# Kernel tuning notes

Hardware: AMD Instinct MI355X
Metric: run time of the kernel (lower is better)

## Reference

```python
import jax, jax.numpy as jnp
import numpy as np

B, N, DEG = 32, 1024, 8
E = B * N * DEG
NT = B * N
F_IN, HID, EDIM, NR, HD = 64, 128, 16, 16, 4
NEG = 0.2  # leaky_relu negative slope (alpha)
K1 = int(np.ceil(0.8 * N))    # 820 kept nodes per graph after pool1
K2 = int(np.ceil(0.8 * K1))   # 656 kept nodes per graph after pool2


def setup_inputs() -> dict:
    key = jax.random.key(0)
    ks = jax.random.split(key, 20)
    nrm = lambda i, shp, s=0.05: jax.random.normal(ks[i], shp, jnp.float32) * s
    x = jax.random.normal(ks[0], (NT, F_IN), jnp.float32)
    off = (jnp.arange(B) * N)[:, None]
    src = (jax.random.randint(ks[1], (B, N * DEG), 0, N) + off).reshape(-1)
    dst = (jax.random.randint(ks[2], (B, N * DEG), 0, N) + off).reshape(-1)
    edge_index = jnp.stack([src, dst]).astype(jnp.int32)
    edge_attr = jax.random.normal(ks[3], (E, EDIM), jnp.float32)
    action = jax.random.normal(ks[4], (B, NR), jnp.float32)
    return dict(
        x=x, edge_attr=edge_attr, action=action,
        W1l=nrm(5, (F_IN, HD * HID)), b1l=jnp.zeros(HD * HID),
        W1r=nrm(6, (F_IN, HD * HID)), b1r=jnp.zeros(HD * HID),
        W1e=nrm(7, (EDIM, HD * HID)), att1=nrm(8, (HD, HID)), bias1=jnp.zeros(HID),
        W2l=nrm(9, (HID, HD * HID)), b2l=jnp.zeros(HD * HID),
        W2r=nrm(10, (HID, HD * HID)), b2r=jnp.zeros(HD * HID),
        W2e=nrm(11, (EDIM, HD * HID)), att2=nrm(12, (HD, HID)), bias2=jnp.zeros(HID),
        p1=nrm(13, (HID,), 0.1), p2=nrm(14, (HID,), 0.1),
        Wf1=nrm(15, (2 * HID + NR, HID)), bf1=jnp.zeros(HID),
        Wf2=nrm(16, (HID, HID)), bf2=jnp.zeros(HID),
        Wf3=nrm(17, (HID, 1), 0.003), bf3=jnp.zeros(1),
        edge_index=edge_index,
    )


def _gatv2(x, edge_index, edge_attr, edge_mask, Wl, bl, Wr, br, We, att, bias):
    # PyG GATv2Conv, concat=False (mean over heads), eval mode (no dropout).
    src, dst = edge_index[0], edge_index[1]
    n = x.shape[0]
    xl = (x @ Wl + bl).reshape(n, HD, HID)   # source transform (x_j)
    xr = (x @ Wr + br).reshape(n, HD, HID)   # target transform (x_i)
    ef = (edge_attr @ We).reshape(-1, HD, HID)
    m = jax.nn.leaky_relu(xl[src] + xr[dst] + ef, NEG)          # [E,H,C]
    logits = jnp.where(edge_mask[:, None], (m * att).sum(-1), -1e9)  # [E,H]
    mx = jax.ops.segment_max(logits, dst, num_segments=n)
    a = jnp.exp(logits - mx[dst])
    den = jax.ops.segment_sum(a, dst, num_segments=n)
    alpha = (a / (den[dst] + 1e-16)) * edge_mask[:, None]       # softmax per dst, masked edges zeroed
    out = jax.ops.segment_sum(xl[src] * alpha[..., None], dst, num_segments=n)
    return out.mean(axis=1) + bias


def _topk(x, node_mask, p, k):
    # PyG TopKPooling: score = x@p/||p||, gate = tanh(score), keep top-k per graph.
    score = (x @ p) / (jnp.linalg.norm(p) + 1e-16)
    gate = jnp.tanh(score)
    s = jnp.where(node_mask, score, -jnp.inf).reshape(B, N)
    idx = jax.lax.top_k(s, k)[1]                                # [B,k]
    keep = jnp.zeros((B, N), bool).at[jnp.arange(B)[:, None], idx].set(True).reshape(-1)
    return x * gate[:, None], keep


def reference(x, edge_attr, action, W1l, b1l, W1r, b1r, W1e, att1, bias1,
              W2l, b2l, W2r, b2r, W2e, att2, bias2, p1, p2,
              Wf1, bf1, Wf2, bf2, Wf3, bf3, edge_index):
    src, dst = edge_index[0], edge_index[1]
    em0 = jnp.ones((E,), bool)
    h = jax.nn.relu(_gatv2(x, edge_index, edge_attr, em0,
                           W1l, b1l, W1r, b1r, W1e, att1, bias1))
    h, keep1 = _topk(h, jnp.ones((NT,), bool), p1, K1)
    em1 = keep1[src] & keep1[dst]
    h = jax.nn.relu(_gatv2(h, edge_index, edge_attr, em1,
                           W2l, b2l, W2r, b2r, W2e, att2, bias2))
    h, keep2 = _topk(h, keep1, p2, K2)
    hb = h.reshape(B, N, HID)
    mb = keep2.reshape(B, N)[..., None]
    gmx = jnp.where(mb, hb, -jnp.inf).max(axis=1)               # global max pool over kept nodes
    gav = (hb * mb).sum(axis=1) / K2                            # global mean pool (K2 kept per graph)
    z = jnp.concatenate([gmx, gav, action], axis=1)             # [B, 2*HID+NR]
    z = jax.nn.relu(z @ Wf1 + bf1)
    z = jax.nn.relu(z @ Wf2 + bf2)
    return z @ Wf3 + bf3
```

## Files before the change

kernel.cpp:

```cpp
#include <hip/hip_runtime.h>
#include <math.h>

#define NTN 32768
#define NBG 32
#define NN  1024
#define EE  262144
#define FIN 64
#define HIDC 128
#define HD  4
#define HC  512
#define EDIM 16
#define NR  16
#define KP1 820
#define KP2 656
#define NKEPT (KP1 * NBG)
#define NEGS 0.2f
#define NPB 2
#define SHIFT 10.0f
#define EPAD (EE + 3 * NTN + 64)

template<int K>
__global__ __launch_bounds__(256) void gemm_node3(const float* __restrict__ A,
                                                  const float* __restrict__ Wl,
                                                  const float* __restrict__ bl,
                                                  const float* __restrict__ Wr,
                                                  const float* __restrict__ br,
                                                  const float* __restrict__ gs,
                                                  const int* __restrict__ ids,
                                                  float* __restrict__ Cl,
                                                  float* __restrict__ Cr) {
    __shared__ float a_s[64][K];
    __shared__ int rid_s[64];
    __shared__ float g_s[64];
    int t = threadIdx.x;
    int rb = blockIdx.x >> 2, cg = blockIdx.x & 3;
    int row0 = rb * 64;
    if (t < 64) {
        int rid = ids ? ids[row0 + t] : (row0 + t);
        rid_s[t] = rid;
        g_s[t] = gs ? tanhf(gs[rid]) : 1.0f;
    }
    __syncthreads();
    for (int i = t; i < 64 * K; i += 256) {
        int r = i / K, k = i % K;
        a_s[r][k] = A[(size_t)rid_s[r] * K + k] * g_s[r];
    }
    __syncthreads();
    int tc = cg * 128 + (t & 63) * 2;
    int rg = (t >> 6) * 16;
    float accl0[16], accl1[16], accr0[16], accr1[16];
    float2 blv = *(const float2*)&bl[tc];
    float2 brv = *(const float2*)&br[tc];
    #pragma unroll
    for (int r = 0; r < 16; r++) { accl0[r] = blv.x; accl1[r] = blv.y; accr0[r] = brv.x; accr1[r] = brv.y; }
    for (int k = 0; k < K; k++) {
        float2 wl = *(const float2*)&Wl[(size_t)k * HC + tc];
        float2 wr = *(const float2*)&Wr[(size_t)k * HC + tc];
        #pragma unroll
        for (int r = 0; r < 16; r++) {
            float a = a_s[rg + r][k];
            accl0[r] += a * wl.x; accl1[r] += a * wl.y;
            accr0[r] += a * wr.x; accr1[r] += a * wr.y;
        }
    }
    for (int r = 0; r < 16; r++) {
        size_t base = (size_t)rid_s[rg + r] * HC + tc;
        *(float2*)&Cl[base] = make_float2(accl0[r], accl1[r]);
        *(float2*)&Cr[base] = make_float2(accr0[r], accr1[r]);
    }
}

__global__ void edge_hist(const int* __restrict__ dst, int* __restrict__ deg) {
    int e = blockIdx.x * 256 + threadIdx.x;
    if (e < EE) atomicAdd(&deg[dst[e]], 1);
}

__global__ __launch_bounds__(1024) void scan_deg(const int* __restrict__ deg,
                                                 int* __restrict__ off, int* __restrict__ cur,
                                                 const float* __restrict__ p1,
                                                 const float* __restrict__ p2,
                                                 float* __restrict__ pn) {
    __shared__ int s[1024];
    int t = threadIdx.x;
    int base = t * 32;
    int local[32];
    int sum = 0;
    #pragma unroll
    for (int i = 0; i < 32; i++) { local[i] = (deg[base + i] + 3) & ~3; sum += local[i]; }
    s[t] = sum;
    for (int o = 1; o < 1024; o <<= 1) {
        __syncthreads();
        int v = (t >= o) ? s[t - o] : 0;
        __syncthreads();
        s[t] += v;
    }
    __syncthreads();
    int run = s[t] - sum;
    #pragma unroll
    for (int i = 0; i < 32; i++) { off[base + i] = run; cur[base + i] = run; run += local[i]; }
    if (t == 1023) off[NTN] = s[1023];
    if (t < 64) {
        float a = p1[t] * p1[t] + p1[t + 64] * p1[t + 64];
        float b = p2[t] * p2[t] + p2[t + 64] * p2[t + 64];
        #pragma unroll
        for (int sft = 32; sft; sft >>= 1) { a += __shfl_xor(a, sft, 64); b += __shfl_xor(b, sft, 64); }
        if (t == 0) { pn[0] = 1.f / (sqrtf(a) + 1e-16f); pn[1] = 1.f / (sqrtf(b) + 1e-16f); }
    }
}

__global__ void edge_scatter(const int* __restrict__ dst, const int* __restrict__ src,
                             const float* __restrict__ ea, int* __restrict__ cur,
                             int* __restrict__ esrc, float* __restrict__ eaP) {
    int e = blockIdx.x * 256 + threadIdx.x;
    if (e < EE) {
        int p = atomicAdd(&cur[dst[e]], 1);
        esrc[p] = src[e];
        const float4* s4 = (const float4*)(ea + (size_t)e * EDIM);
        float4* d4 = (float4*)(eaP + (size_t)p * EDIM);
        d4[0] = s4[0]; d4[1] = s4[1]; d4[2] = s4[2]; d4[3] = s4[3];
    }
}

__global__ void pad_fill(const int* __restrict__ cur, const int* __restrict__ off,
                         int* __restrict__ esrc, float* __restrict__ eaP) {
    int d = blockIdx.x * 256 + threadIdx.x;
    if (d < NTN) {
        int p0 = cur[d], p1 = off[d + 1];
        float4 z = make_float4(0.f, 0.f, 0.f, 0.f);
        for (int p = p0; p < p1; p++) {
            esrc[p] = -1;
            float4* d4 = (float4*)(eaP + (size_t)p * EDIM);
            d4[0] = z; d4[1] = z; d4[2] = z; d4[3] = z;
        }
    }
}

__global__ __launch_bounds__(256) void gat_dst(
        const float* __restrict__ xl, const float* __restrict__ xr,
        const float* __restrict__ eaP, const float* __restrict__ We,
        const float* __restrict__ att, const float* __restrict__ bias,
        const float* __restrict__ pvec, const float* __restrict__ pnInv,
        const int* __restrict__ esrc, const int* __restrict__ off,
        const int* __restrict__ keep,
        float* __restrict__ out, float* __restrict__ score, int nblk) {
    int bid = blockIdx.x;
    int swz = (bid & 7) * (nblk >> 3) + (bid >> 3);
    int d0 = swz * NPB;
    int t = threadIdx.x;
    int w = t >> 6, lane = t & 63;
    int c = w * HIDC + lane * 2;
    __shared__ float red[NPB][HC];
    __shared__ float red2[NPB][HIDC];
    float we0[EDIM], we1[EDIM];
    #pragma unroll
    for (int k = 0; k < EDIM; k++) {
        we0[k] = We[k * HC + c];
        we1[k] = We[k * HC + c + 1];
    }
    float at0 = att[c], at1 = att[c + 1];
    const float* xlc = xl + c;

    for (int n = 0; n < NPB; n++) {
        int d = d0 + n;
        float denA = 0.f, aA0 = 0.f, aA1 = 0.f;
        float denB = 0.f, aB0 = 0.f, aB1 = 0.f;
        bool live = (keep == nullptr) || (keep[d] != 0);
        if (live) {
            float2 xrv = *(const float2*)&xr[((size_t)d << 9) + c];
            int e0 = __builtin_amdgcn_readfirstlane(off[d]);
            int e1 = __builtin_amdgcn_readfirstlane(off[d + 1]);
            for (int ei = e0; ei < e1; ei += 4) {
                int s[4]; float msk[4]; float2 xv[4]; float p[4];
                #pragma unroll
                for (int j = 0; j < 4; j++) {
                    int sv = esrc[ei + j];
                    int sc = sv < 0 ? 0 : sv;
                    float mk = (sv >= 0) ? 1.f : 0.f;
                    if (keep && sv >= 0 && !keep[sc]) mk = 0.f;
                    s[j] = sc; msk[j] = mk;
                }
                #pragma unroll
                for (int j = 0; j < 4; j++) xv[j] = *(const float2*)&xlc[(size_t)s[j] << 9];
                #pragma unroll
                for (int j = 0; j < 4; j++) {
                    const float* eap = eaP + (size_t)(ei + j) * EDIM;
                    float ef0 = 0.f, ef1 = 0.f;
                    #pragma unroll
                    for (int k = 0; k < EDIM; k++) {
                        float e = eap[k];
                        ef0 += e * we0[k]; ef1 += e * we1[k];
                    }
                    float v0 = xv[j].x + xrv.x + ef0; v0 = v0 > 0.f ? v0 : NEGS * v0;
                    float v1 = xv[j].y + xrv.y + ef1; v1 = v1 > 0.f ? v1 : NEGS * v1;
                    p[j] = v0 * at0 + v1 * at1;
                }
                #pragma unroll
                for (int sft = 32; sft; sft >>= 1) {
                    #pragma unroll
                    for (int j = 0; j < 4; j++) p[j] += __shfl_xor(p[j], sft, 64);
                }
                float w0 = msk[0] * __expf(p[0] - SHIFT);
                float w1 = msk[1] * __expf(p[1] - SHIFT);
                float w2 = msk[2] * __expf(p[2] - SHIFT);
                float w3 = msk[3] * __expf(p[3] - SHIFT);
                denA += w0; aA0 += w0 * xv[0].x; aA1 += w0 * xv[0].y;
                denB += w1; aB0 += w1 * xv[1].x; aB1 += w1 * xv[1].y;
                denA += w2; aA0 += w2 * xv[2].x; aA1 += w2 * xv[2].y;
                denB += w3; aB0 += w3 * xv[3].x; aB1 += w3 * xv[3].y;
            }
        }
        float inv = 1.f / (denA + denB + 1e-16f);
        red[n][c] = (aA0 + aB0) * inv;
        red[n][c + 1] = (aA1 + aB1) * inv;
    }
    __syncthreads();
    {
        int n2 = t >> 7, tc = t & 127;
        float v = (red[n2][tc] + red[n2][tc + 128] + red[n2][tc + 256] + red[n2][tc + 384]) * 0.25f
                  + bias[tc];
        v = fmaxf(v, 0.f);
        out[((size_t)(d0 + n2) << 7) + tc] = v;
        red2[n2][tc] = v * pvec[tc];
    }
    __syncthreads();
    if (t < 128) {
        int n3 = t >> 6, l2 = t & 63;
        float sv = red2[n3][l2] + red2[n3][l2 + 64];
        #pragma unroll
        for (int sft = 32; sft; sft >>= 1) sv += __shfl_xor(sv, sft, 64);
        if (l2 == 0) score[d0 + n3] = sv * pnInv[0];
    }
}

__global__ __launch_bounds__(512) void topk_sel(const float* __restrict__ score,
                                                const int* __restrict__ mask, int k,
                                                int* __restrict__ keep, int* __restrict__ klist) {
    __shared__ float v[NN];
    __shared__ short id[NN];
    int g = blockIdx.x, t = threadIdx.x;
    for (int i = t; i < NN; i += 512) {
        int n = g * NN + i;
        bool mk = mask ? (mask[n] != 0) : true;
        v[i] = mk ? score[n] : -INFINITY;
        id[i] = (short)i;
    }
    __syncthreads();
    for (int kk = 2; kk <= NN; kk <<= 1) {
        for (int j = kk >> 1; j > 0; j >>= 1) {
            #pragma unroll 2
            for (int i = t; i < NN; i += 512) {
                int ixj = i ^ j;
                if (ixj > i) {
                    bool up = ((i & kk) == 0);
                    float a = v[i], b2 = v[ixj];
                    short ia = id[i], ib = id[ixj];
                    bool aFirst = (a > b2) || (a == b2 && ia < ib);
                    if (up ? !aFirst : aFirst) { v[i] = b2; v[ixj] = a; id[i] = ib; id[ixj] = ia; }
                }
            }
            __syncthreads();
        }
    }
    for (int i = t; i < NN; i += 512) {
        int kp = (i < k) ? 1 : 0;
        keep[g * NN + id[i]] = kp;
        if (klist && kp) klist[g * k + i] = g * NN + id[i];
    }
}

__global__ __launch_bounds__(512) void tail(const float* __restrict__ score,
                                            const int* __restrict__ mask,
                                            const float* __restrict__ h,
                                            const float* __restrict__ action,
                                            const float* __restrict__ Wf1, const float* __restrict__ bf1,
                                            const float* __restrict__ Wf2, const float* __restrict__ bf2,
                                            const float* __restrict__ Wf3, const float* __restrict__ bf3,
                                            float* __restrict__ out) {
    int g = blockIdx.x, t = threadIdx.x;
    __shared__ float v[NN];
    __shared__ short id[NN];
    __shared__ float gt_s[NN];
    __shared__ char kp_s[NN];
    __shared__ float smx[4][HIDC], ssm[4][HIDC];
    __shared__ float zs[2 * HIDC + NR], z1[HIDC], z2[HIDC], rr[HIDC];
    for (int i = t; i < NN; i += 512) {
        int n = g * NN + i;
        bool mk = (mask[n] != 0);
        v[i] = mk ? score[n] : -INFINITY;
        id[i] = (short)i;
        kp_s[i] = 0;
        gt_s[i] = 0.f;
    }
    __syncthreads();
    for (int kk = 2; kk <= NN; kk <<= 1) {
        for (int j = kk >> 1; j > 0; j >>= 1) {
            #pragma unroll 2
            for (int i = t; i < NN; i += 512) {
                int ixj = i ^ j;
                if (ixj > i) {
                    bool up = ((i & kk) == 0);
                    float a = v[i], b2 = v[ixj];
                    short ia = id[i], ib = id[ixj];
                    bool aFirst = (a > b2) || (a == b2 && ia < ib);
                    if (up ? !aFirst : aFirst) { v[i] = b2; v[ixj] = a; id[i] = ib; id[ixj] = ia; }
                }
            }
            __syncthreads();
        }
    }
    for (int i = t; i < NN; i += 512) {
        if (i < KP2) {
            int nid = id[i];
            kp_s[nid] = 1;
            gt_s[nid] = tanhf(score[g * NN + nid]);
        }
    }
    __syncthreads();
    int c = t & 127, ch = t >> 7;
    float mx = -INFINITY, sm = 0.f;
    for (int n = ch * 256; n < ch * 256 + 256; n++) {
        if (kp_s[n]) {
            float hv = h[(size_t)(g * NN + n) * HIDC + c] * gt_s[n];
            mx = fmaxf(mx, hv);
            sm += hv;
        }
    }
    smx[ch][c] = mx; ssm[ch][c] = sm;
    __syncthreads();
    if (t < HIDC) {
        mx = fmaxf(fmaxf(smx[0][t], smx[1][t]), fmaxf(smx[2][t], smx[3][t]));
        sm = ssm[0][t] + ssm[1][t] + ssm[2][t] + ssm[3][t];
        zs[t] = mx;
        zs[HIDC + t] = sm / (float)KP2;
        if (t < NR) zs[2 * HIDC + t] = action[g * NR + t];
    }
    __syncthreads();
    if (t < HIDC) {
        float a = bf1[t];
        for (int k = 0; k < 2 * HIDC + NR; k++) a += zs[k] * Wf1[(size_t)k * HIDC + t];
        z1[t] = fmaxf(a, 0.f);
    }
    __syncthreads();
    if (t < HIDC) {
        float a = bf2[t];
        for (int k = 0; k < HIDC; k++) a += z1[k] * Wf2[(size_t)k * HIDC + t];
        z2[t] = fmaxf(a, 0.f);
        rr[t] = z2[t] * Wf3[t];
    }
    __syncthreads();
    for (int s = 64; s; s >>= 1) {
        if (t < s) rr[t] += rr[t + s];
        __syncthreads();
    }
    if (t == 0) out[g] = rr[0] + bf3[0];
}

extern "C" void kernel_launch(void* const* d_in, const int* in_sizes, int n_in,
                              void* d_out, int out_size, void* d_ws, size_t ws_size,
                              hipStream_t stream) {
    const float* x    = (const float*)d_in[0];
    const float* ea   = (const float*)d_in[1];
    const float* act  = (const float*)d_in[2];
    const float* W1l  = (const float*)d_in[3];
    const float* b1l  = (const float*)d_in[4];
    const float* W1r  = (const float*)d_in[5];
    const float* b1r  = (const float*)d_in[6];
    const float* W1e  = (const float*)d_in[7];
    const float* att1 = (const float*)d_in[8];
    const float* bias1= (const float*)d_in[9];
    const float* W2l  = (const float*)d_in[10];
    const float* b2l  = (const float*)d_in[11];
    const float* W2r  = (const float*)d_in[12];
    const float* b2r  = (const float*)d_in[13];
    const float* W2e  = (const float*)d_in[14];
    const float* att2 = (const float*)d_in[15];
    const float* bias2= (const float*)d_in[16];
    const float* p1   = (const float*)d_in[17];
    const float* p2   = (const float*)d_in[18];
    const float* Wf1  = (const float*)d_in[19];
    const float* bf1  = (const float*)d_in[20];
    const float* Wf2  = (const float*)d_in[21];
    const float* bf2  = (const float*)d_in[22];
    const float* Wf3  = (const float*)d_in[23];
    const float* bf3  = (const float*)d_in[24];
    const int*   eix  = (const int*)d_in[25];
    const int* srcA = eix;
    const int* dstA = eix + EE;

    float* ws    = (float*)d_ws;
    float* xl    = ws;
    float* xr    = xl + (size_t)NTN * HC;
    float* h     = xr + (size_t)NTN * HC;
    float* score1= h + (size_t)NTN * HIDC;
    float* score2= score1 + NTN;
    float* pn    = score2 + NTN;
    int* keep1 = (int*)(pn + 2);
    int* klist = keep1 + NTN;
    int* deg   = klist + NKEPT;
    int* off   = deg + NTN;
    int* cur   = off + NTN + 1;
    int* esrc  = cur + NTN;
    float* eaP  = (float*)(esrc + EPAD);

    hipMemsetAsync(deg, 0, NTN * sizeof(int), stream);
    edge_hist<<<EE / 256, 256, 0, stream>>>(dstA, deg);
    scan_deg<<<1, 1024, 0, stream>>>(deg, off, cur, p1, p2, pn);
    edge_scatter<<<EE / 256, 256, 0, stream>>>(dstA, srcA, ea, cur, esrc, eaP);
    pad_fill<<<NTN / 256, 256, 0, stream>>>(cur, off, esrc, eaP);

    gemm_node3<FIN><<<(NTN / 64) * 4, 256, 0, stream>>>(x, W1l, b1l, W1r, b1r, nullptr, nullptr, xl, xr);
    gat_dst<<<NTN / NPB, 256, 0, stream>>>(xl, xr, eaP, W1e, att1, bias1, p1, pn, esrc, off, nullptr, h, score1, NTN / NPB);

    topk_sel<<<NBG, 512, 0, stream>>>(score1, nullptr, KP1, keep1, klist);

    gemm_node3<HIDC><<<(NKEPT / 64) * 4, 256, 0, stream>>>(h, W2l, b2l, W2r, b2r, score1, klist, xl, xr);
    gat_dst<<<NTN / NPB, 256, 0, stream>>>(xl, xr, eaP, W2e, att2, bias2, p2, pn + 1, esrc, off, keep1, h, score2, NTN / NPB);

    tail<<<NBG, 512, 0, stream>>>(score2, keep1, h, act,
                                  Wf1, bf1, Wf2, bf2, Wf3, bf3, (float*)d_out);
}
```

Baseline: 600.6 us.

## Build per-graph CSR in shared memory, precompute masked sources, use transpose-reduce for logits

Replaces the global histogram, single-block scan, scatter and pad-fill kernels with one per-graph CSR build that uses shared-memory atomics, plus a separate permutation pass for edge attributes. Padding is dropped: tail slots are clamped and masked instead. A precomputed esrc2 array folds the keep1 source mask in before layer 2, so the gather loop no longer reads keep. The four per-edge logit reductions now share one transpose-style shuffle tree instead of four full butterflies, with float4 edge-attribute loads and 32-bit index math. This costs an extra masking kernel and a perm buffer.

```diff
diff --git a/kernel.cpp b/kernel.cpp
--- a/kernel.cpp
+++ b/kernel.cpp
@@ -4,6 +4,7 @@
 #define NTN 32768
 #define NBG 32
 #define NN  1024
+#define EPG 8192
 #define EE  262144
 #define FIN 64
 #define HIDC 128
@@ -17,7 +18,6 @@
 #define NEGS 0.2f
 #define NPB 2
 #define SHIFT 10.0f
-#define EPAD (EE + 3 * NTN + 64)
 
 template<int K>
 __global__ __launch_bounds__(256) void gemm_node3(const float* __restrict__ A,
@@ -70,71 +70,70 @@
     }
 }
 
-__global__ void edge_hist(const int* __restrict__ dst, int* __restrict__ deg) {
-    int e = blockIdx.x * 256 + threadIdx.x;
-    if (e < EE) atomicAdd(&deg[dst[e]], 1);
-}
-
-__global__ __launch_bounds__(1024) void scan_deg(const int* __restrict__ deg,
-                                                 int* __restrict__ off, int* __restrict__ cur,
-                                                 const float* __restrict__ p1,
-                                                 const float* __restrict__ p2,
-                                                 float* __restrict__ pn) {
-    __shared__ int s[1024];
-    int t = threadIdx.x;
-    int base = t * 32;
-    int local[32];
-    int sum = 0;
+__global__ __launch_bounds__(1024) void csr_build(const int* __restrict__ dst,
+                                                  const int* __restrict__ src,
+                                                  int* __restrict__ off,
+                                                  int* __restrict__ esrc,
+                                                  int* __restrict__ perm,
+                                                  const float* __restrict__ p1,
+                                                  const float* __restrict__ p2,
+                                                  float* __restrict__ pn) {
+    int g = blockIdx.x, t = threadIdx.x;
+    __shared__ int degS[NN];
+    __shared__ int scanS[NN];
+    __shared__ int curS[NN];
+    degS[t] = 0;
+    __syncthreads();
+    int eb = g * EPG;
     #pragma unroll
-    for (int i = 0; i < 32; i++) { local[i] = (deg[base + i] + 3) & ~3; sum += local[i]; }
-    s[t] = sum;
-    for (int o = 1; o < 1024; o <<= 1) {
+    for (int i = t; i < EPG; i += 1024) atomicAdd(&degS[dst[eb + i] - g * NN], 1);
+    __syncthreads();
+    int dg = degS[t];
+    scanS[t] = dg;
+    for (int o = 1; o < NN; o <<= 1) {
         __syncthreads();
-        int v = (t >= o) ? s[t - o] : 0;
+        int v = (t >= o) ? scanS[t - o] : 0;
         __syncthreads();
-        s[t] += v;
-    }
-    __syncthreads();
-    int run = s[t] - sum;
-    #pragma unroll
-    for (int i = 0; i < 32; i++) { off[base + i] = run; cur[base + i] = run; run += local[i]; }
-    if (t == 1023) off[NTN] = s[1023];
-    if (t < 64) {
+        scanS[t] += v;
+    }
+    __syncthreads();
+    int excl = scanS[t] - dg;
+    off[g * NN + t] = eb + excl;
+    curS[t] = excl;
+    if (g == NBG - 1 && t == NN - 1) off[NTN] = EE;
+    if (g == 0 && t < 64) {
         float a = p1[t] * p1[t] + p1[t + 64] * p1[t + 64];
         float b = p2[t] * p2[t] + p2[t + 64] * p2[t + 64];
         #pragma unroll
         for (int sft = 32; sft; sft >>= 1) { a += __shfl_xor(a, sft, 64); b += __shfl_xor(b, sft, 64); }
         if (t == 0) { pn[0] = 1.f / (sqrtf(a) + 1e-16f); pn[1] = 1.f / (sqrtf(b) + 1e-16f); }
     }
-}
-
-__global__ void edge_scatter(const int* __restrict__ dst, const int* __restrict__ src,
-                             const float* __restrict__ ea, int* __restrict__ cur,
-                             int* __restrict__ esrc, float* __restrict__ eaP) {
-    int e = blockIdx.x * 256 + threadIdx.x;
-    if (e < EE) {
-        int p = atomicAdd(&cur[dst[e]], 1);
+    __syncthreads();
+    #pragma unroll
+    for (int i = t; i < EPG; i += 1024) {
+        int e = eb + i;
+        int ld = dst[e] - g * NN;
+        int p = eb + atomicAdd(&curS[ld], 1);
         esrc[p] = src[e];
-        const float4* s4 = (const float4*)(ea + (size_t)e * EDIM);
-        float4* d4 = (float4*)(eaP + (size_t)p * EDIM);
-        d4[0] = s4[0]; d4[1] = s4[1]; d4[2] = s4[2]; d4[3] = s4[3];
-    }
-}
-
-__global__ void pad_fill(const int* __restrict__ cur, const int* __restrict__ off,
-                         int* __restrict__ esrc, float* __restrict__ eaP) {
-    int d = blockIdx.x * 256 + threadIdx.x;
-    if (d < NTN) {
-        int p0 = cur[d], p1 = off[d + 1];
-        float4 z = make_float4(0.f, 0.f, 0.f, 0.f);
-        for (int p = p0; p < p1; p++) {
-            esrc[p] = -1;
-            float4* d4 = (float4*)(eaP + (size_t)p * EDIM);
-            d4[0] = z; d4[1] = z; d4[2] = z; d4[3] = z;
-        }
-    }
-}
-
+        perm[p] = e;
+    }
+}
+
+__global__ void ea_permute(const int* __restrict__ perm, const float* __restrict__ ea,
+                           float* __restrict__ eaP) {
+    int id = blockIdx.x * 256 + threadIdx.x;
+    int p = id >> 2, q = id & 3;
+    ((float4*)eaP)[p * 4 + q] = ((const float4*)ea)[perm[p] * 4 + q];
+}
+
+__global__ void esrc_mask(const int* __restrict__ esrc, const int* __restrict__ keep,
+                          int* __restrict__ esrc2) {
+    int i = blockIdx.x * 256 + threadIdx.x;
+    int sv = esrc[i];
+    esrc2[i] = keep[sv] ? sv : -1;
+}
+
+template<bool L2>
 __global__ __launch_bounds__(256) void gat_dst(
         const float* __restrict__ xl, const float* __restrict__ xr,
         const float* __restrict__ eaP, const float* __restrict__ We,
@@ -164,49 +163,61 @@
         int d = d0 + n;
         float denA = 0.f, aA0 = 0.f, aA1 = 0.f;
         float denB = 0.f, aB0 = 0.f, aB1 = 0.f;
-        bool live = (keep == nullptr) || (keep[d] != 0);
+        bool live = !L2 || (keep[d] != 0);
         if (live) {
-            float2 xrv = *(const float2*)&xr[((size_t)d << 9) + c];
+            float2 xrv = *(const float2*)&xr[((unsigned)d << 9) + (unsigned)c];
             int e0 = __builtin_amdgcn_readfirstlane(off[d]);
             int e1 = __builtin_amdgcn_readfirstlane(off[d + 1]);
+            int last = e1 - 1;
             for (int ei = e0; ei < e1; ei += 4) {
-                int s[4]; float msk[4]; float2 xv[4]; float p[4];
+                float mk[4]; float2 xv[4]; float p[4]; int slc[4];
                 #pragma unroll
                 for (int j = 0; j < 4; j++) {
-                    int sv = esrc[ei + j];
-                    int sc = sv < 0 ? 0 : sv;
-                    float mk = (sv >= 0) ? 1.f : 0.f;
-                    if (keep && sv >= 0 && !keep[sc]) mk = 0.f;
-                    s[j] = sc; msk[j] = mk;
+                    int sl = ei + j;
+                    slc[j] = sl <= last ? sl : last;
+                    int sv = esrc[slc[j]];
+                    float m = (sl <= last && sv >= 0) ? 1.f : 0.f;
+                    int sidx = sv >= 0 ? sv : 0;
+                    mk[j] = m;
+                    xv[j] = *(const float2*)(xlc + ((unsigned)sidx << 9));
                 }
                 #pragma unroll
-                for (int j = 0; j < 4; j++) xv[j] = *(const float2*)&xlc[(size_t)s[j] << 9];
-                #pragma unroll
                 for (int j = 0; j < 4; j++) {
-                    const float* eap = eaP + (size_t)(ei + j) * EDIM;
+                    const float4* eap = (const float4*)eaP + ((unsigned)slc[j] << 2);
+                    float4 E0 = eap[0], E1 = eap[1], E2 = eap[2], E3 = eap[3];
+                    float ev[16] = {E0.x, E0.y, E0.z, E0.w, E1.x, E1.y, E1.z, E1.w,
+                                    E2.x, E2.y, E2.z, E2.w, E3.x, E3.y, E3.z, E3.w};
                     float ef0 = 0.f, ef1 = 0.f;
                     #pragma unroll
-                    for (int k = 0; k < EDIM; k++) {
-                        float e = eap[k];
-                        ef0 += e * we0[k]; ef1 += e * we1[k];
-                    }
+                    for (int k = 0; k < EDIM; k++) { ef0 += ev[k] * we0[k]; ef1 += ev[k] * we1[k]; }
                     float v0 = xv[j].x + xrv.x + ef0; v0 = v0 > 0.f ? v0 : NEGS * v0;
                     float v1 = xv[j].y + xrv.y + ef1; v1 = v1 > 0.f ? v1 : NEGS * v1;
                     p[j] = v0 * at0 + v1 * at1;
                 }
-                #pragma unroll
-                for (int sft = 32; sft; sft >>= 1) {
-                    #pragma unroll
-                    for (int j = 0; j < 4; j++) p[j] += __shfl_xor(p[j], sft, 64);
-                }
-                float w0 = msk[0] * __expf(p[0] - SHIFT);
-                float w1 = msk[1] * __expf(p[1] - SHIFT);
-                float w2 = msk[2] * __expf(p[2] - SHIFT);
-                float w3 = msk[3] * __expf(p[3] - SHIFT);
-                denA += w0; aA0 += w0 * xv[0].x; aA1 += w0 * xv[0].y;
-                denB += w1; aB0 += w1 * xv[1].x; aB1 += w1 * xv[1].y;
-                denA += w2; aA0 += w2 * xv[2].x; aA1 += w2 * xv[2].y;
-                denB += w3; aB0 += w3 * xv[3].x; aB1 += w3 * xv[3].y;
+                bool o1 = (lane & 1), o2 = (lane & 2);
+                float a0 = o1 ? p[1] : p[0], b0 = o1 ? p[0] : p[1];
+                float q0 = a0 + __shfl_xor(b0, 1, 64);
+                float a1 = o1 ? p[3] : p[2], b1 = o1 ? p[2] : p[3];
+                float q1 = a1 + __shfl_xor(b1, 1, 64);
+                float a2 = o2 ? q1 : q0, b2 = o2 ? q0 : q1;
+                float r = a2 + __shfl_xor(b2, 2, 64);
+                r += __shfl_xor(r, 4, 64);
+                r += __shfl_xor(r, 8, 64);
+                r += __shfl_xor(r, 16, 64);
+                r += __shfl_xor(r, 32, 64);
+                float s0 = __shfl(r, 0, 64);
+                float s1 = __shfl(r, 1, 64);
+                float s2 = __shfl(r, 2, 64);
+                float s3 = __shfl(r, 3, 64);
+                float w0 = mk[0] * __expf(s0 - SHIFT);
+                float w1 = mk[1] * __expf(s1 - SHIFT);
+                float w2 = mk[2] * __expf(s2 - SHIFT);
+                float w3 = mk[3] * __expf(s3 - SHIFT);
+                denA += w0 + w2; denB += w1 + w3;
+                aA0 += w0 * xv[0].x; aA1 += w0 * xv[0].y;
+                aB0 += w1 * xv[1].x; aB1 += w1 * xv[1].y;
+                aA0 += w2 * xv[2].x; aA1 += w2 * xv[2].y;
+                aB0 += w3 * xv[3].x; aB1 += w3 * xv[3].y;
             }
         }
         float inv = 1.f / (denA + denB + 1e-16f);
@@ -219,7 +230,7 @@
         float v = (red[n2][tc] + red[n2][tc + 128] + red[n2][tc + 256] + red[n2][tc + 384]) * 0.25f
                   + bias[tc];
         v = fmaxf(v, 0.f);
-        out[((size_t)(d0 + n2) << 7) + tc] = v;
+        out[((unsigned)(d0 + n2) << 7) + (unsigned)tc] = v;
         red2[n2][tc] = v * pvec[tc];
     }
     __syncthreads();
@@ -396,25 +407,23 @@
     float* pn    = score2 + NTN;
     int* keep1 = (int*)(pn + 2);
     int* klist = keep1 + NTN;
-    int* deg   = klist + NKEPT;
-    int* off   = deg + NTN;
-    int* cur   = off + NTN + 1;
-    int* esrc  = cur + NTN;
-    float* eaP  = (float*)(esrc + EPAD);
-
-    hipMemsetAsync(deg, 0, NTN * sizeof(int), stream);
-    edge_hist<<<EE / 256, 256, 0, stream>>>(dstA, deg);
-    scan_deg<<<1, 1024, 0, stream>>>(deg, off, cur, p1, p2, pn);
-    edge_scatter<<<EE / 256, 256, 0, stream>>>(dstA, srcA, ea, cur, esrc, eaP);
-    pad_fill<<<NTN / 256, 256, 0, stream>>>(cur, off, esrc, eaP);
+    int* off   = klist + NKEPT;
+    int* esrc  = off + NTN + 1;
+    int* esrc2 = esrc + EE;
+    int* perm  = esrc2 + EE;
+    float* eaP = (float*)(perm + EE);
+
+    csr_build<<<NBG, 1024, 0, stream>>>(dstA, srcA, off, esrc, perm, p1, p2, pn);
+    ea_permute<<<EE * 4 / 256, 256, 0, stream>>>(perm, ea, eaP);
 
     gemm_node3<FIN><<<(NTN / 64) * 4, 256, 0, stream>>>(x, W1l, b1l, W1r, b1r, nullptr, nullptr, xl, xr);
-    gat_dst<<<NTN / NPB, 256, 0, stream>>>(xl, xr, eaP, W1e, att1, bias1, p1, pn, esrc, off, nullptr, h, score1, NTN / NPB);
+    gat_dst<false><<<NTN / NPB, 256, 0, stream>>>(xl, xr, eaP, W1e, att1, bias1, p1, pn, esrc, off, nullptr, h, score1, NTN / NPB);
 
     topk_sel<<<NBG, 512, 0, stream>>>(score1, nullptr, KP1, keep1, klist);
 
+    esrc_mask<<<EE / 256, 256, 0, stream>>>(esrc, keep1, esrc2);
     gemm_node3<HIDC><<<(NKEPT / 64) * 4, 256, 0, stream>>>(h, W2l, b2l, W2r, b2r, score1, klist, xl, xr);
-    gat_dst<<<NTN / NPB, 256, 0, stream>>>(xl, xr, eaP, W2e, att2, bias2, p2, pn + 1, esrc, off, keep1, h, score2, NTN / NPB);
+    gat_dst<true><<<NTN / NPB, 256, 0, stream>>>(xl, xr, eaP, W2e, att2, bias2, p2, pn + 1, esrc2, off, keep1, h, score2, NTN / NPB);
 
     tail<<<NBG, 512, 0, stream>>>(score2, keep1, h, act,
                                   Wf1, bf1, Wf2, bf2, Wf3, bf3, (float*)d_out);
```

New measurement: 748.3 us. 24.6% more time.
